# Kernel optimization log

Hardware: AMD Instinct MI355X
Metric: run time of the kernel (lower is better)

## Reference

```python
import jax, jax.numpy as jnp
import numpy as np

HIDDEN = 1024
D_MEM = 256
BATCH = 4
SEQ = 1024
EPS = 1e-6


def elu_plus_one(x):
    # F.elu(x) + 1 == exp(x) for x<0, x+1 for x>=0 (positive feature map)
    return jnp.where(x > 0, x + 1.0, jnp.exp(x))


def setup_inputs() -> dict:
    key = jax.random.key(0)
    ks = jax.random.split(key, 8)
    hidden_states = jax.random.normal(ks[0], (BATCH, SEQ, HIDDEN), dtype=jnp.float32)
    s = 1.0 / np.sqrt(HIDDEN)
    w_q = jax.random.normal(ks[1], (D_MEM, HIDDEN), dtype=jnp.float32) * s
    w_k = jax.random.normal(ks[2], (D_MEM, HIDDEN), dtype=jnp.float32) * s
    w_v = jax.random.normal(ks[3], (D_MEM, HIDDEN), dtype=jnp.float32) * s
    w_o = jax.random.normal(ks[4], (HIDDEN, D_MEM), dtype=jnp.float32) * (1.0 / np.sqrt(D_MEM))
    gate = jnp.zeros((1,), dtype=jnp.float32)
    # nonzero persistent memory state so retrieval path is exercised
    memory = jax.random.normal(ks[5], (D_MEM, D_MEM), dtype=jnp.float32) * 0.1
    memory_norm = jax.random.uniform(ks[6], (D_MEM,), dtype=jnp.float32) * 10.0 + 1.0
    return {
        "hidden_states": hidden_states,
        "w_q": w_q, "w_k": w_k, "w_v": w_v, "w_o": w_o,
        "gate": gate, "memory": memory, "memory_norm": memory_norm,
    }


def _retrieve(sigma_x, memory, memory_norm):
    # [b,s,d] @ [d,d] -> [b,s,d], normalized by sigma_x @ memory_norm
    a_unnorm = jnp.matmul(sigma_x, memory)
    norm = jnp.clip(jnp.matmul(sigma_x, memory_norm), EPS, None)[..., None]
    out = a_unnorm / norm
    # torch: if memory_norm.sum() < 1e-6 -> zeros
    return jnp.where(memory_norm.sum() < EPS, jnp.zeros_like(out), out)


def reference(hidden_states, w_q, w_k, w_v, w_o, gate, memory, memory_norm):
    b, s, _ = hidden_states.shape
    q = jnp.einsum('bsh,dh->bsd', hidden_states, w_q)
    k = jnp.einsum('bsh,dh->bsd', hidden_states, w_k)
    v = jnp.einsum('bsh,dh->bsd', hidden_states, w_v)

    sigma_q = elu_plus_one(q)
    sigma_k = elu_plus_one(k)

    # --- retrieval from compressive memory ---
    memory_output = _retrieve(sigma_q, memory, memory_norm)

    # --- causal linear attention within segment (cumsum form, as in source) ---
    kv = jnp.einsum('bsd,bse->bsde', sigma_k, v)          # [b,s,d,d]
    kv_cumsum = jnp.cumsum(kv, axis=1)                     # [b,s,d,d]
    k_cumsum = jnp.cumsum(sigma_k, axis=1)                 # [b,s,d]
    numerator = jnp.einsum('bsd,bsde->bse', sigma_q, kv_cumsum)
    denominator = jnp.clip(jnp.einsum('bsd,bsd->bs', sigma_q, k_cumsum), EPS, None)[..., None]
    local_output = numerator / denominator

    g = jax.nn.sigmoid(gate[0])
    combined = g * memory_output + (1.0 - g) * local_output
    output = jnp.einsum('bsd,hd->bsh', combined, w_o)

    # --- delta-rule memory update (detached in torch) ---
    retrieved_unnorm = jnp.matmul(sigma_k, memory)
    norm = jnp.clip(jnp.matmul(sigma_k, memory_norm), EPS, None)[..., None]
    delta_v = v - retrieved_unnorm / norm
    memory_update = jnp.einsum('bsd,bse->de', sigma_k, delta_v) / (b * s)
    new_memory = jax.lax.stop_gradient(memory + memory_update)
    z_update = sigma_k.sum(axis=(0, 1)) / b
    new_memory_norm = jax.lax.stop_gradient(memory_norm + z_update)

    return output, new_memory, new_memory_norm
```

## Files before the change

kernel.cpp:

```cpp
#include <hip/hip_runtime.h>


#define HIDDEN 1024
#define DMEM 256
#define BATCH 4
#define SEQ 1024
#define MTOT (BATCH * SEQ)
#define CHUNK 128
#define NCH (SEQ / CHUNK)
#define NCHT (BATCH * NCH)
#define EPSF 1e-6f

typedef __bf16 bf16x8 __attribute__((ext_vector_type(8)));
typedef __bf16 bf16x4 __attribute__((ext_vector_type(4)));
typedef float f32x4 __attribute__((ext_vector_type(4)));

#define GL_LDS(g, l)                                                                   \
  __builtin_amdgcn_global_load_lds((const __attribute__((address_space(1))) void*)(g), \
                                   (__attribute__((address_space(3))) void*)(l), 16, 0, 0)

__device__ __forceinline__ float elu1(float x) { return x > 0.f ? x + 1.f : __expf(x); }

__device__ __forceinline__ void stage128(const __bf16* p, long ld, int k0, __bf16* sm,
                                         int wave) {
// ... 15 lines not shown
    stage128(aptr, lda, k0, smA, wave);
    stage128(bptr, ldb, k0, smB, wave);
    __syncthreads();
#pragma unroll
    for (int h = 0; h < 2; ++h) {
      bf16x8 aF[4], bF[4];
#pragma unroll
      for (int i = 0; i < 4; ++i)
        aF[i] = *reinterpret_cast<const bf16x8*>(smA + h * 4096 +
                                                 (wr * 64 + i * 16 + l16) * 32 + quad * 8);
#pragma unroll
      for (int j = 0; j < 4; ++j)
        bF[j] = *reinterpret_cast<const bf16x8*>(smB + h * 4096 +
                                                 (wc * 64 + j * 16 + l16) * 32 + quad * 8);
#pragma unroll
      for (int i = 0; i < 4; ++i)
#pragma unroll
        for (int j = 0; j < 4; ++j)
          acc[i][j] = __builtin_amdgcn_mfma_f32_16x16x32_bf16(aF[i], bF[j], acc[i][j], 0, 0, 0);
    }
    __syncthreads();
  }
}

__device__ __forceinline__ void gemm64_bk64(const __bf16* aptr, const __bf16* bptr, long ldb,
                                            int klen, __bf16* smA, __bf16* smB, int wave,
                                            int wr, int wc, int quad, int l16,
                                            f32x4 (&acc)[2][4]) {
  for (int k0 = 0; k0 < klen; k0 += 64) {
    stage64(aptr, k0, smA, wave);
    stage128(bptr, ldb, k0, smB, wave);
    __syncthreads();
#pragma unroll
    for (int h = 0; h < 2; ++h) {
      bf16x8 aF[2], bF[4];
#pragma unroll
      for (int i = 0; i < 2; ++i)
        aF[i] = *reinterpret_cast<const bf16x8*>(smA + h * 2048 +
                                                 (wr * 32 + i * 16 + l16) * 32 + quad * 8);
#pragma unroll
      for (int j = 0; j < 4; ++j)
        bF[j] = *reinterpret_cast<const bf16x8*>(smB + h * 4096 +
                                                 (wc * 64 + j * 16 + l16) * 32 + quad * 8);
#pragma unroll
      for (int i = 0; i < 2; ++i)
#pragma unroll
        for (int j = 0; j < 4; ++j)
          acc[i][j] = __builtin_amdgcn_mfma_f32_16x16x32_bf16(aF[i], bF[j], acc[i][j], 0, 0, 0);
    }
    __syncthreads();
  }
}

__global__ void kprep(const float* __restrict__ hs, const float* __restrict__ wq,
                      const float* __restrict__ wk, const float* __restrict__ wv,
                      const float* __restrict__ wo, const float* __restrict__ mem,
                      __bf16* __restrict__ hsb, __bf16* __restrict__ wqkvb,
                      __bf16* __restrict__ wob, __bf16* __restrict__ memT,
                      float* __restrict__ out) {
  __shared__ float s[64][65];
  int b = blockIdx.x, tid = threadIdx.x;
  if (b < 4096) {
    int i = b * 256 + tid;
    float4 f = reinterpret_cast<const float4*>(hs)[i];
    bf16x4 h = {(__bf16)f.x, (__bf16)f.y, (__bf16)f.z, (__bf16)f.w};
    reinterpret_cast<bf16x4*>(hsb)[i] = h;
  } else if (b < 5120) {
    int y = (b - 4096) >> 8;
    const float* src = (y == 0) ? wq : (y == 1) ? wk : (y == 2) ? wv : wo;
    __bf16* dst = (y < 3) ? wqkvb + (size_t)y * (DMEM * HIDDEN) : wob;
    int i = ((b - 4096) & 255) * 256 + tid;
    float4 f = reinterpret_cast<const float4*>(src)[i];
    bf16x4 h = {(__bf16)f.x, (__bf16)f.y, (__bf16)f.z, (__bf16)f.w};
    reinterpret_cast<bf16x4*>(dst)[i] = h;
  } else if (b < 5136) {
    int t = b - 5120;
    int bx = t & 3, by = t >> 2;
    int r0 = tid >> 6, col = tid & 63;
#pragma unroll
    for (int it = 0; it < 16; ++it) {
      int row = it * 4 + r0;
      s[row][col] = mem[(size_t)(by * 64 + row) * DMEM + bx * 64 + col];
    }
    __syncthreads();
#pragma unroll
    for (int it = 0; it < 16; ++it) {
      int row = it * 4 + r0;
      memT[(size_t)(bx * 64 + row) * DMEM + by * 64 + col] = (__bf16)s[col][row];
    }
  } else {
    int g = (b - 5136) * 256 + tid;
    reinterpret_cast<float4*>(out + (size_t)MTOT * HIDDEN)[g] =
        reinterpret_cast<const float4*>(mem)[g];
  }
}

__global__ __launch_bounds__(256) void k1_qkv_mfma(
    const __bf16* __restrict__ X, const __bf16* __restrict__ W, __bf16* __restrict__ sqb,
    __bf16* __restrict__ skb, __bf16* __restrict__ skT, __bf16* __restrict__ vT) {
  __shared__ __bf16 As[4096];
  __shared__ __bf16 Bs[8192];
  int tid = threadIdx.x;
  int lane = tid & 63, wave = tid >> 6;
  int m0 = blockIdx.x * 64;
  int by = blockIdx.y;
  int wsel = by >> 1, n0 = (by & 1) * 128;
  const __bf16* aptr = X + (size_t)(m0 + (tid >> 2)) * HIDDEN + ((tid & 3) << 3);
  const __bf16* bptr = W + (size_t)(by * 128 + (tid >> 2)) * HIDDEN + ((tid & 3) << 3);
  int wr = wave >> 1, wc = wave & 1, quad = lane >> 4, l16 = lane & 15;
  f32x4 acc[2][4] = {};
  gemm64_bk64(aptr, bptr, HIDDEN, HIDDEN, As, Bs, wave, wr, wc, quad, l16, acc);
#pragma unroll
  for (int i = 0; i < 2; ++i)
#pragma unroll
    for (int j = 0; j < 4; ++j) {
      int mb = m0 + wr * 32 + i * 16 + quad * 4;
      int n = n0 + wc * 64 + j * 16 + l16;
      if (wsel == 0) {
#pragma unroll
        for (int r = 0; r < 4; ++r) sqb[(size_t)(mb + r) * DMEM + n] = (__bf16)elu1(acc[i][j][r]);
      } else if (wsel == 1) {
        bf16x4 t;
#pragma unroll
        for (int r = 0; r < 4; ++r) {
          float v = elu1(acc[i][j][r]);
          skb[(size_t)(mb + r) * DMEM + n] = (__bf16)v;
          t[r] = (__bf16)v;
        }
        *reinterpret_cast<bf16x4*>(skT + (size_t)n * MTOT + mb) = t;
      } else {
        bf16x4 t;
#pragma unroll
        for (int r = 0; r < 4; ++r) t[r] = (__bf16)acc[i][j][r];
        *reinterpret_cast<bf16x4*>(vT + (size_t)n * MTOT + mb) = t;
      }
    }
}

__global__ __launch_bounds__(256) void kC(const __bf16* __restrict__ vT,
                                          const __bf16* __restrict__ skT,
                                          const __bf16* __restrict__ sqb,
                                          const __bf16* __restrict__ skb,
                                          __bf16* __restrict__ kvcT, __bf16* __restrict__ scb,
                                          float* __restrict__ ksc) {
  __shared__ __bf16 As[4096];
  __shared__ __bf16 Bs[8192];
  int tid = threadIdx.x;
  int c = blockIdx.x;
  int y = blockIdx.y;
  if (y == 10) {
    int d = tid;
    float s = 0.f;
    for (int i = 0; i < CHUNK; ++i) s += (float)skb[(size_t)(c * CHUNK + i) * DMEM + d];
    ksc[c * DMEM + d] = s;
    return;
  }
  int lane = tid & 63, wave = tid >> 6;
  int wr = wave >> 1, wc = wave & 1, quad = lane >> 4, l16 = lane & 15;
  if (y < 8) {
    int e0 = (y >> 1) * 64, d0 = (y & 1) * 128;
    const __bf16* aptr = vT + (size_t)(e0 + (tid >> 2)) * MTOT + c * CHUNK + ((tid & 3) << 3);
    const __bf16* bptr = skT + (size_t)(d0 + (tid >> 2)) * MTOT + c * CHUNK + ((tid & 3) << 3);
    f32x4 acc[2][4] = {};
    gemm64_bk64(aptr, bptr, MTOT, CHUNK, As, Bs, wave, wr, wc, quad, l16, acc);
#pragma unroll
    for (int i = 0; i < 2; ++i)
#pragma unroll
      for (int j = 0; j < 4; ++j)
#pragma unroll
        for (int r = 0; r < 4; ++r) {
          int e = e0 + wr * 32 + i * 16 + quad * 4 + r;
          int d = d0 + wc * 64 + j * 16 + l16;
          kvcT[(size_t)c * DMEM * DMEM + (size_t)e * DMEM + d] = (__bf16)acc[i][j][r];
        }
  } else {
    int i0 = (y - 8) * 64;
    const __bf16* aptr = sqb + (size_t)(c * CHUNK + i0 + (tid >> 2)) * DMEM + ((tid & 3) << 3);
    const __bf16* bptr = skb + (size_t)(c * CHUNK + (tid >> 2)) * DMEM + ((tid & 3) << 3);
    f32x4 acc[2][4] = {};
    gemm64_bk64(aptr, bptr, DMEM, DMEM, As, Bs, wave, wr, wc, quad, l16, acc);
#pragma unroll
    for (int i = 0; i < 2; ++i)
#pragma unroll
      for (int j = 0; j < 4; ++j)
#pragma unroll
        for (int r = 0; r < 4; ++r) {
          int ii = i0 + wr * 32 + i * 16 + quad * 4 + r;
          int jj = wc * 64 + j * 16 + l16;
          scb[(size_t)c * CHUNK * CHUNK + (size_t)ii * CHUNK + jj] =
              (jj <= ii) ? (__bf16)acc[i][j][r] : (__bf16)0.f;
        }
  }
}

__global__ __launch_bounds__(256) void kD(const __bf16* __restrict__ kvcT,
                                          __bf16* __restrict__ kvpT,
                                          const float* __restrict__ ksc,
                                          const __bf16* __restrict__ scb,
                                          const __bf16* __restrict__ sqb,
                                          const __bf16* __restrict__ skb,
                                          const float* __restrict__ mnorm,
                                          float* __restrict__ den, float* __restrict__ qn,
                                          float* __restrict__ kn) {
  int vt = blockIdx.x;
  int tid = threadIdx.x;
  if (vt < 128) {
    int batch = vt >> 5;
    size_t idx8 = (size_t)(((vt & 31) * 256 + tid)) * 8;
    float run[8] = {};
    for (int c = 0; c < NCH; ++c) {
      size_t off = (size_t)(batch * NCH + c) * DMEM * DMEM + idx8;
      bf16x8 t = *reinterpret_cast<const bf16x8*>(kvcT + off);
      bf16x8 o;
#pragma unroll
      for (int r = 0; r < 8; ++r) o[r] = (__bf16)run[r];
      *reinterpret_cast<bf16x8*>(kvpT + off) = o;
#pragma unroll
      for (int r = 0; r < 8; ++r) run[r] += (float)t[r];
    }
  } else {
    int wave = tid >> 6, lane = tid & 63;
    int m = (vt - 128) * 4 + wave;
    int c = m >> 7;
    int i = m & 127;
    int cb = c & ~7;
    float s_sc = 0.f, s_d2 = 0.f, s_qn = 0.f, s_kn = 0.f;
    for (int j = lane; j < CHUNK; j += 64)
      s_sc += (float)scb[(size_t)c * CHUNK * CHUNK + (size_t)i * CHUNK + j];
    for (int d = lane; d < DMEM; d += 64) {
      float q = (float)sqb[(size_t)m * DMEM + d];
      float k = (float)skb[(size_t)m * DMEM + d];
      float kp = 0.f;
      for (int cc = cb; cc < c; ++cc) kp += ksc[cc * DMEM + d];
      s_d2 += q * kp;
      s_qn += q * mnorm[d];
      s_kn += k * mnorm[d];
    }
#pragma unroll
    for (int off = 32; off > 0; off >>= 1) {
      s_sc += __shfl_down(s_sc, off);
      s_d2 += __shfl_down(s_d2, off);
      s_qn += __shfl_down(s_qn, off);
      s_kn += __shfl_down(s_kn, off);
    }
    if (lane == 0) {
      den[m] = s_sc + s_d2;
      qn[m] = s_qn;
      kn[m] = s_kn;
    }
  }
}

__global__ __launch_bounds__(256) void kE(const __bf16* __restrict__ scb,
                                          const __bf16* __restrict__ sqb,
                                          const __bf16* __restrict__ skb,
                                          const __bf16* __restrict__ vT,
                                          const __bf16* __restrict__ kvpT,
                                          const __bf16* __restrict__ memT,
                                          const float* __restrict__ den,
                                          const float* __restrict__ qn,
                                          const float* __restrict__ kn,
                                          const float* __restrict__ gate,
                                          const float* __restrict__ mnorm,
                                          __bf16* __restrict__ combb, __bf16* __restrict__ dvT) {
  __shared__ __bf16 As[4096];
  __shared__ __bf16 B1s[8192];
  __shared__ __bf16 B2s[8192];
  __shared__ float warr[4];
  int tid = threadIdx.x;
  int lane = tid & 63, wave = tid >> 6;
  int wr = wave >> 1, wc = wave & 1, quad = lane >> 4, l16 = lane & 15;
  int bid = blockIdx.x;
  if (bid < 128) {
    float mv = mnorm[tid];
#pragma unroll
    for (int off = 32; off > 0; off >>= 1) mv += __shfl_down(mv, off);
    if (lane == 0) warr[wave] = mv;
    __syncthreads();
    float fl = ((warr[0] + warr[1] + warr[2] + warr[3]) < EPSF) ? 0.f : 1.f;
    __syncthreads();
    int c = bid >> 2, yy = bid & 3;
    int i0 = (yy >> 1) * 64, e0 = (yy & 1) * 128;
    f32x4 acc_loc[2][4] = {};
    f32x4 acc_mem[2][4] = {};
    {
      const __bf16* aptr =
          scb + (size_t)c * CHUNK * CHUNK + (size_t)(i0 + (tid >> 2)) * CHUNK + ((tid & 3) << 3);
      const __bf16* bptr = vT + (size_t)(e0 + (tid >> 2)) * MTOT + c * CHUNK + ((tid & 3) << 3);
      gemm64_bk64(aptr, bptr, MTOT, CHUNK, As, B1s, wave, wr, wc, quad, l16, acc_loc);
    }
    {
      const __bf16* aptr = sqb + (size_t)(c * CHUNK + i0 + (tid >> 2)) * DMEM + ((tid & 3) << 3);
      const __bf16* b1ptr =
          kvpT + (size_t)c * DMEM * DMEM + (size_t)(e0 + (tid >> 2)) * DMEM + ((tid & 3) << 3);
      const __bf16* b2ptr = memT + (size_t)(e0 + (tid >> 2)) * DMEM + ((tid & 3) << 3);
      for (int k0 = 0; k0 < DMEM; k0 += 64) {
        stage64(aptr, k0, As, wave);
        stage128(b1ptr, DMEM, k0, B1s, wave);
        stage128(b2ptr, DMEM, k0, B2s, wave);
        __syncthreads();
#pragma unroll
        for (int h = 0; h < 2; ++h) {
          bf16x8 aF[2], b1F[4], b2F[4];
#pragma unroll
          for (int i = 0; i < 2; ++i)
            aF[i] = *reinterpret_cast<const bf16x8*>(As + h * 2048 +
                                                     (wr * 32 + i * 16 + l16) * 32 + quad * 8);
#pragma unroll
          for (int j = 0; j < 4; ++j) {
            b1F[j] = *reinterpret_cast<const bf16x8*>(B1s + h * 4096 +
                                                      (wc * 64 + j * 16 + l16) * 32 + quad * 8);
            b2F[j] = *reinterpret_cast<const bf16x8*>(B2s + h * 4096 +
                                                      (wc * 64 + j * 16 + l16) * 32 + quad * 8);
          }
#pragma unroll
          for (int i = 0; i < 2; ++i)
#pragma unroll
            for (int j = 0; j < 4; ++j) {
              acc_loc[i][j] =
                  __builtin_amdgcn_mfma_f32_16x16x32_bf16(aF[i], b1F[j], acc_loc[i][j], 0, 0, 0);
              acc_mem[i][j] =
                  __builtin_amdgcn_mfma_f32_16x16x32_bf16(aF[i], b2F[j], acc_mem[i][j], 0, 0, 0);
            }
        }
        __syncthreads();
      }
    }
    float g = 1.f / (1.f + __expf(-gate[0]));
#pragma unroll
    for (int i = 0; i < 2; ++i) {
      int mb = c * CHUNK + i0 + wr * 32 + i * 16 + quad * 4;
      float dn[4], qv[4];
#pragma unroll
      for (int r = 0; r < 4; ++r) {
        dn[r] = fmaxf(den[mb + r], EPSF);
        qv[r] = fmaxf(qn[mb + r], EPSF);
      }
#pragma unroll
      for (int j = 0; j < 4; ++j) {
        int e = e0 + wc * 64 + j * 16 + l16;
#pragma unroll
        for (int r = 0; r < 4; ++r) {
          float comb = g * fl * acc_mem[i][j][r] / qv[r] + (1.f - g) * acc_loc[i][j][r] / dn[r];
          combb[(size_t)(mb + r) * DMEM + e] = (__bf16)comb;
        }
      }
    }
  } else {
    int t = bid - 128;
    int m0 = (t >> 1) * 64, n0 = (t & 1) * 128;
    const __bf16* aptr = skb + (size_t)(m0 + (tid >> 2)) * DMEM + ((tid & 3) << 3);
    const __bf16* bptr = memT + (size_t)(n0 + (tid >> 2)) * DMEM + ((tid & 3) << 3);
    f32x4 acc[2][4] = {};
    gemm64_bk64(aptr, bptr, DMEM, DMEM, As, B1s, wave, wr, wc, quad, l16, acc);
#pragma unroll
    for (int i = 0; i < 2; ++i) {
      int mb = m0 + wr * 32 + i * 16 + quad * 4;
      float kv[4];
#pragma unroll
      for (int r = 0; r < 4; ++r) kv[r] = fmaxf(kn[mb + r], EPSF);
#pragma unroll
      for (int j = 0; j < 4; ++j) {
        int n = n0 + wc * 64 + j * 16 + l16;
        bf16x4 vv = *reinterpret_cast<const bf16x4*>(vT + (size_t)n * MTOT + mb);
        bf16x4 tt;
#pragma unroll
        for (int r = 0; r < 4; ++r) tt[r] = (__bf16)((float)vv[r] - acc[i][j][r] / kv[r]);
        *reinterpret_cast<bf16x4*>(dvT + (size_t)n * MTOT + mb) = tt;
      }
    }
  }
}

__global__ __launch_bounds__(256) void kF(const __bf16* __restrict__ combb,
                                          const __bf16* __restrict__ wob,
                                          const __bf16* __restrict__ skT,
                                          const __bf16* __restrict__ dvT,
                                          const float* __restrict__ ksc,
                                          const float* __restrict__ mnorm,
                                          float* __restrict__ out) {
  __shared__ __bf16 As[8192];
  __shared__ __bf16 Bs[8192];
  int tid = threadIdx.x;
  int bid = blockIdx.x;
  if (bid == 384) {
    int d = tid;
    float s = 0.f;
    for (int c = 0; c < NCHT; ++c) s += ksc[c * DMEM + d];
    out[(size_t)MTOT * HIDDEN + DMEM * DMEM + d] = mnorm[d] + s * (1.f / (float)BATCH);
    return;
  }
  int lane = tid & 63, wave = tid >> 6;
  int wr = wave >> 1, wc = wave & 1, quad = lane >> 4, l16 = lane & 15;
  if (bid < 256) {
    int m0 = (bid & 31) * 128, by = bid >> 5;
    const __bf16* aptr = combb + (size_t)(m0 + (tid >> 2)) * DMEM + ((tid & 3) << 3);
    const __bf16* bptr = wob + (size_t)(by * 128 + (tid >> 2)) * DMEM + ((tid & 3) << 3);
    f32x4 acc[4][4] = {};
    gemm128_bk64(aptr, DMEM, bptr, DMEM, DMEM, As, Bs, wave, wr, wc, quad, l16, acc);
#pragma unroll
    for (int i = 0; i < 4; ++i)
#pragma unroll
      for (int j = 0; j < 4; ++j)
#pragma unroll
        for (int r = 0; r < 4; ++r) {
          int m = m0 + wr * 64 + i * 16 + quad * 4 + r;
          int n = by * 128 + wc * 64 + j * 16 + l16;
          out[(size_t)m * HIDDEN + n] = acc[i][j][r];
        }
  } else {
    int t = bid - 256;
    int kbase = (t >> 3) * 256;
    int yy = t & 7;
    int d0 = (yy >> 1) * 64, e0 = (yy & 1) * 128;
    const __bf16* aptr = skT + (size_t)(d0 + (tid >> 2)) * MTOT + kbase + ((tid & 3) << 3);
    const __bf16* bptr = dvT + (size_t)(e0 + (tid >> 2)) * MTOT + kbase + ((tid & 3) << 3);
    f32x4 acc[2][4] = {};
    gemm64_bk64(aptr, bptr, MTOT, 256, As, Bs, wave, wr, wc, quad, l16, acc);
    float* base = out + (size_t)MTOT * HIDDEN;
#pragma unroll
    for (int i = 0; i < 2; ++i)
#pragma unroll
      for (int j = 0; j < 4; ++j)
#pragma unroll
        for (int r = 0; r < 4; ++r) {
          int d = d0 + wr * 32 + i * 16 + quad * 4 + r;
          int e = e0 + wc * 64 + j * 16 + l16;
          atomicAdd(&base[(size_t)d * DMEM + e], acc[i][j][r] * (1.f / (float)MTOT));
        }
  }
}

extern "C" void kernel_launch(void* const* d_in, const int* in_sizes, int n_in,
                              void* d_out, int out_size, void* d_ws, size_t ws_size,
                              hipStream_t stream) {
  const float* hs = (const float*)d_in[0];
  const float* wq = (const float*)d_in[1];
  const float* wk = (const float*)d_in[2];
  const float* wv = (const float*)d_in[3];
  const float* wo = (const float*)d_in[4];
  const float* gate = (const float*)d_in[5];
  const float* mem = (const float*)d_in[6];
  const float* mnorm = (const float*)d_in[7];
  float* out = (float*)d_out;
  float* ws = (float*)d_ws;

  float* ksc = ws;
  float* den = ksc + 8192;
  float* qn = den + 4096;
  float* kn = qn + 4096;
  __bf16* kvcT = (__bf16*)(ws + 20480);
  __bf16* hsb = kvcT + (size_t)NCHT * DMEM * DMEM;
  __bf16* wqkvb = hsb + (size_t)MTOT * HIDDEN;
  __bf16* wob = wqkvb + (size_t)3 * DMEM * HIDDEN;
  __bf16* memT = wob + (size_t)HIDDEN * DMEM;
  __bf16* sqb = memT + (size_t)DMEM * DMEM;
  __bf16* skb = sqb + (size_t)MTOT * DMEM;
  __bf16* skT = skb + (size_t)MTOT * DMEM;
  __bf16* vT = skT + (size_t)MTOT * DMEM;
  __bf16* scb = vT + (size_t)MTOT * DMEM;
  __bf16* kvpT = scb + (size_t)NCHT * CHUNK * CHUNK;
  __bf16* combb = kvpT + (size_t)NCHT * DMEM * DMEM;
  __bf16* dvT = combb + (size_t)MTOT * DMEM;

  kprep<<<dim3(5152), 256, 0, stream>>>(hs, wq, wk, wv, wo, mem, hsb, wqkvb, wob, memT, out);
  k1_qkv_mfma<<<dim3(64, 6), 256, 0, stream>>>(hsb, wqkvb, sqb, skb, skT, vT);
  kC<<<dim3(NCHT, 11), 256, 0, stream>>>(vT, skT, sqb, skb, kvcT, scb, ksc);
  kD<<<dim3(1152), 256, 0, stream>>>(kvcT, kvpT, ksc, scb, sqb, skb, mnorm, den, qn, kn);
  kE<<<dim3(256), 256, 0, stream>>>(scb, sqb, skb, vT, kvpT, memT, den, qn, kn, gate, mnorm,
                                    combb, dvT);
  kF<<<dim3(385), 256, 0, stream>>>(combb, wob, skT, dvT, ksc, mnorm, out);
}
```

Before: 139.2 us.

## Fuse scan and normalizer kernels into neighbours, drop kvp prefix buffer

Removes the separate prefix-scan/denominator kernel. The delta-v computation (with its k-norm reduction done in shared memory) moves into the chunk kernel. The retrieval kernel now computes its own denominators and accumulates prior chunk KV products via repeated GEMMs over earlier chunks instead of reading a precomputed prefix. The memory-update GEMM moves into the retrieval launch, and the output projection becomes its own kernel. This cuts one launch and the global round trips for den/qn/kn/kvpT, but adds redundant per-block reductions and up to seven extra GEMMs for late chunks. The kprep grid size also changes.

```diff
diff --git a/kernel.cpp b/kernel.cpp
--- a/kernel.cpp
+++ b/kernel.cpp
@@ -176,14 +176,17 @@
     }
 }
 
-__global__ __launch_bounds__(256) void kC(const __bf16* __restrict__ vT,
-                                          const __bf16* __restrict__ skT,
-                                          const __bf16* __restrict__ sqb,
-                                          const __bf16* __restrict__ skb,
-                                          __bf16* __restrict__ kvcT, __bf16* __restrict__ scb,
-                                          float* __restrict__ ksc) {
+__global__ __launch_bounds__(256) void kC2(const __bf16* __restrict__ vT,
+                                           const __bf16* __restrict__ skT,
+                                           const __bf16* __restrict__ sqb,
+                                           const __bf16* __restrict__ skb,
+                                           const __bf16* __restrict__ memT,
+                                           const float* __restrict__ mnorm,
+                                           __bf16* __restrict__ kvcT, __bf16* __restrict__ scb,
+                                           float* __restrict__ ksc, __bf16* __restrict__ dvT) {
   __shared__ __bf16 As[4096];
   __shared__ __bf16 Bs[8192];
+  __shared__ float knl[64];
   int tid = threadIdx.x;
   int c = blockIdx.x;
   int y = blockIdx.y;
@@ -212,7 +215,7 @@
           int d = d0 + wc * 64 + j * 16 + l16;
           kvcT[(size_t)c * DMEM * DMEM + (size_t)e * DMEM + d] = (__bf16)acc[i][j][r];
         }
-  } else {
+  } else if (y < 10) {
     int i0 = (y - 8) * 64;
     const __bf16* aptr = sqb + (size_t)(c * CHUNK + i0 + (tid >> 2)) * DMEM + ((tid & 3) << 3);
     const __bf16* bptr = skb + (size_t)(c * CHUNK + (tid >> 2)) * DMEM + ((tid & 3) << 3);
@@ -229,87 +232,69 @@
           scb[(size_t)c * CHUNK * CHUNK + (size_t)ii * CHUNK + jj] =
               (jj <= ii) ? (__bf16)acc[i][j][r] : (__bf16)0.f;
         }
-  }
-}
-
-__global__ __launch_bounds__(256) void kD(const __bf16* __restrict__ kvcT,
-                                          __bf16* __restrict__ kvpT,
-                                          const float* __restrict__ ksc,
-                                          const __bf16* __restrict__ scb,
-                                          const __bf16* __restrict__ sqb,
-                                          const __bf16* __restrict__ skb,
-                                          const float* __restrict__ mnorm,
-                                          float* __restrict__ den, float* __restrict__ qn,
-                                          float* __restrict__ kn) {
-  int vt = blockIdx.x;
-  int tid = threadIdx.x;
-  if (vt < 128) {
-    int batch = vt >> 5;
-    size_t idx8 = (size_t)(((vt & 31) * 256 + tid)) * 8;
-    float run[8] = {};
-    for (int c = 0; c < NCH; ++c) {
-      size_t off = (size_t)(batch * NCH + c) * DMEM * DMEM + idx8;
-      bf16x8 t = *reinterpret_cast<const bf16x8*>(kvcT + off);
-      bf16x8 o;
-#pragma unroll
-      for (int r = 0; r < 8; ++r) o[r] = (__bf16)run[r];
-      *reinterpret_cast<bf16x8*>(kvpT + off) = o;
-#pragma unroll
-      for (int r = 0; r < 8; ++r) run[r] += (float)t[r];
-    }
   } else {
-    int wave = tid >> 6, lane = tid & 63;
-    int m = (vt - 128) * 4 + wave;
-    int c = m >> 7;
-    int i = m & 127;
-    int cb = c & ~7;
-    float s_sc = 0.f, s_d2 = 0.f, s_qn = 0.f, s_kn = 0.f;
-    for (int j = lane; j < CHUNK; j += 64)
-      s_sc += (float)scb[(size_t)c * CHUNK * CHUNK + (size_t)i * CHUNK + j];
-    for (int d = lane; d < DMEM; d += 64) {
-      float q = (float)sqb[(size_t)m * DMEM + d];
-      float k = (float)skb[(size_t)m * DMEM + d];
-      float kp = 0.f;
-      for (int cc = cb; cc < c; ++cc) kp += ksc[cc * DMEM + d];
-      s_d2 += q * kp;
-      s_qn += q * mnorm[d];
-      s_kn += k * mnorm[d];
-    }
-#pragma unroll
-    for (int off = 32; off > 0; off >>= 1) {
-      s_sc += __shfl_down(s_sc, off);
-      s_d2 += __shfl_down(s_d2, off);
-      s_qn += __shfl_down(s_qn, off);
-      s_kn += __shfl_down(s_kn, off);
-    }
-    if (lane == 0) {
-      den[m] = s_sc + s_d2;
-      qn[m] = s_qn;
-      kn[m] = s_kn;
-    }
-  }
-}
-
-__global__ __launch_bounds__(256) void kE(const __bf16* __restrict__ scb,
-                                          const __bf16* __restrict__ sqb,
-                                          const __bf16* __restrict__ skb,
-                                          const __bf16* __restrict__ vT,
-                                          const __bf16* __restrict__ kvpT,
-                                          const __bf16* __restrict__ memT,
-                                          const float* __restrict__ den,
-                                          const float* __restrict__ qn,
-                                          const float* __restrict__ kn,
-                                          const float* __restrict__ gate,
-                                          const float* __restrict__ mnorm,
-                                          __bf16* __restrict__ combb, __bf16* __restrict__ dvT) {
+    int t = (y - 11) * 32 + c;
+    int m0 = (t >> 1) * 64, n0 = (t & 1) * 128;
+    for (int rr = 0; rr < 16; ++rr) {
+      int m = m0 + wave * 16 + rr;
+      float s = 0.f;
+      for (int d = lane; d < DMEM; d += 64) s += (float)skb[(size_t)m * DMEM + d] * mnorm[d];
+#pragma unroll
+      for (int off = 32; off > 0; off >>= 1) s += __shfl_down(s, off);
+      if (lane == 0) knl[wave * 16 + rr] = s;
+    }
+    __syncthreads();
+    const __bf16* aptr = skb + (size_t)(m0 + (tid >> 2)) * DMEM + ((tid & 3) << 3);
+    const __bf16* bptr = memT + (size_t)(n0 + (tid >> 2)) * DMEM + ((tid & 3) << 3);
+    f32x4 acc[2][4] = {};
+    gemm64_bk64(aptr, bptr, DMEM, DMEM, As, Bs, wave, wr, wc, quad, l16, acc);
+#pragma unroll
+    for (int i = 0; i < 2; ++i) {
+      int rel = wr * 32 + i * 16 + quad * 4;
+      float kv[4];
+#pragma unroll
+      for (int r = 0; r < 4; ++r) kv[r] = fmaxf(knl[rel + r], EPSF);
+#pragma unroll
+      for (int j = 0; j < 4; ++j) {
+        int n = n0 + wc * 64 + j * 16 + l16;
+        bf16x4 vv = *reinterpret_cast<const bf16x4*>(vT + (size_t)n * MTOT + m0 + rel);
+        bf16x4 tt;
+#pragma unroll
+        for (int r = 0; r < 4; ++r) tt[r] = (__bf16)((float)vv[r] - acc[i][j][r] / kv[r]);
+        *reinterpret_cast<bf16x4*>(dvT + (size_t)n * MTOT + m0 + rel) = tt;
+      }
+    }
+  }
+}
+
+__global__ __launch_bounds__(256) void kE2(const __bf16* __restrict__ scb,
+                                           const __bf16* __restrict__ sqb,
+                                           const __bf16* __restrict__ vT,
+                                           const __bf16* __restrict__ kvcT,
+                                           const __bf16* __restrict__ memT,
+                                           const __bf16* __restrict__ skT,
+                                           const __bf16* __restrict__ dvT,
+                                           const float* __restrict__ ksc,
+                                           const float* __restrict__ gate,
+                                           const float* __restrict__ mnorm,
+                                           __bf16* __restrict__ combb,
+                                           float* __restrict__ out) {
   __shared__ __bf16 As[4096];
-  __shared__ __bf16 B1s[8192];
-  __shared__ __bf16 B2s[8192];
+  __shared__ __bf16 Bs[8192];
+  __shared__ float denl[64];
+  __shared__ float qnl[64];
   __shared__ float warr[4];
   int tid = threadIdx.x;
+  int bid = blockIdx.x;
   int lane = tid & 63, wave = tid >> 6;
   int wr = wave >> 1, wc = wave & 1, quad = lane >> 4, l16 = lane & 15;
-  int bid = blockIdx.x;
+  if (bid == 256) {
+    int d = tid;
+    float s = 0.f;
+    for (int c = 0; c < NCHT; ++c) s += ksc[c * DMEM + d];
+    out[(size_t)MTOT * HIDDEN + DMEM * DMEM + d] = mnorm[d] + s * (1.f / (float)BATCH);
+    return;
+  }
   if (bid < 128) {
     float mv = mnorm[tid];
 #pragma unroll
@@ -317,63 +302,62 @@
     if (lane == 0) warr[wave] = mv;
     __syncthreads();
     float fl = ((warr[0] + warr[1] + warr[2] + warr[3]) < EPSF) ? 0.f : 1.f;
-    __syncthreads();
     int c = bid >> 2, yy = bid & 3;
     int i0 = (yy >> 1) * 64, e0 = (yy & 1) * 128;
+    int cb = c & ~7;
+    for (int rr = 0; rr < 16; ++rr) {
+      int row = wave * 16 + rr;
+      int m = c * CHUNK + i0 + row;
+      float s_sc = 0.f, s_d2 = 0.f, s_qn = 0.f;
+      for (int j = lane; j < CHUNK; j += 64)
+        s_sc += (float)scb[(size_t)c * CHUNK * CHUNK + (size_t)(i0 + row) * CHUNK + j];
+      for (int d = lane; d < DMEM; d += 64) {
+        float q = (float)sqb[(size_t)m * DMEM + d];
+        float kp = 0.f;
+        for (int cc = cb; cc < c; ++cc) kp += ksc[cc * DMEM + d];
+        s_d2 += q * kp;
+        s_qn += q * mnorm[d];
+      }
+#pragma unroll
+      for (int off = 32; off > 0; off >>= 1) {
+        s_sc += __shfl_down(s_sc, off);
+        s_d2 += __shfl_down(s_d2, off);
+        s_qn += __shfl_down(s_qn, off);
+      }
+      if (lane == 0) {
+        denl[row] = s_sc + s_d2;
+        qnl[row] = s_qn;
+      }
+    }
+    __syncthreads();
     f32x4 acc_loc[2][4] = {};
     f32x4 acc_mem[2][4] = {};
     {
       const __bf16* aptr =
           scb + (size_t)c * CHUNK * CHUNK + (size_t)(i0 + (tid >> 2)) * CHUNK + ((tid & 3) << 3);
       const __bf16* bptr = vT + (size_t)(e0 + (tid >> 2)) * MTOT + c * CHUNK + ((tid & 3) << 3);
-      gemm64_bk64(aptr, bptr, MTOT, CHUNK, As, B1s, wave, wr, wc, quad, l16, acc_loc);
+      gemm64_bk64(aptr, bptr, MTOT, CHUNK, As, Bs, wave, wr, wc, quad, l16, acc_loc);
+    }
+    const __bf16* aq = sqb + (size_t)(c * CHUNK + i0 + (tid >> 2)) * DMEM + ((tid & 3) << 3);
+    for (int j = cb; j < c; ++j) {
+      const __bf16* bj =
+          kvcT + (size_t)j * DMEM * DMEM + (size_t)(e0 + (tid >> 2)) * DMEM + ((tid & 3) << 3);
+      gemm64_bk64(aq, bj, DMEM, DMEM, As, Bs, wave, wr, wc, quad, l16, acc_loc);
     }
     {
-      const __bf16* aptr = sqb + (size_t)(c * CHUNK + i0 + (tid >> 2)) * DMEM + ((tid & 3) << 3);
-      const __bf16* b1ptr =
-          kvpT + (size_t)c * DMEM * DMEM + (size_t)(e0 + (tid >> 2)) * DMEM + ((tid & 3) << 3);
-      const __bf16* b2ptr = memT + (size_t)(e0 + (tid >> 2)) * DMEM + ((tid & 3) << 3);
-      for (int k0 = 0; k0 < DMEM; k0 += 64) {
-        stage64(aptr, k0, As, wave);
-        stage128(b1ptr, DMEM, k0, B1s, wave);
-        stage128(b2ptr, DMEM, k0, B2s, wave);
-        __syncthreads();
-#pragma unroll
-        for (int h = 0; h < 2; ++h) {
-          bf16x8 aF[2], b1F[4], b2F[4];
-#pragma unroll
-          for (int i = 0; i < 2; ++i)
-            aF[i] = *reinterpret_cast<const bf16x8*>(As + h * 2048 +
-                                                     (wr * 32 + i * 16 + l16) * 32 + quad * 8);
-#pragma unroll
-          for (int j = 0; j < 4; ++j) {
-            b1F[j] = *reinterpret_cast<const bf16x8*>(B1s + h * 4096 +
-                                                      (wc * 64 + j * 16 + l16) * 32 + quad * 8);
-            b2F[j] = *reinterpret_cast<const bf16x8*>(B2s + h * 4096 +
-                                                      (wc * 64 + j * 16 + l16) * 32 + quad * 8);
-          }
-#pragma unroll
-          for (int i = 0; i < 2; ++i)
-#pragma unroll
-            for (int j = 0; j < 4; ++j) {
-              acc_loc[i][j] =
-                  __builtin_amdgcn_mfma_f32_16x16x32_bf16(aF[i], b1F[j], acc_loc[i][j], 0, 0, 0);
-              acc_mem[i][j] =
-                  __builtin_amdgcn_mfma_f32_16x16x32_bf16(aF[i], b2F[j], acc_mem[i][j], 0, 0, 0);
-            }
-        }
-        __syncthreads();
-      }
+      const __bf16* bm = memT + (size_t)(e0 + (tid >> 2)) * DMEM + ((tid & 3) << 3);
+      gemm64_bk64(aq, bm, DMEM, DMEM, As, Bs, wave, wr, wc, quad, l16, acc_mem);
     }
     float g = 1.f / (1.f + __expf(-gate[0]));
 #pragma unroll
     for (int i = 0; i < 2; ++i) {
-      int mb = c * CHUNK + i0 + wr * 32 + i * 16 + quad * 4;
+      int rel = wr * 32 + i * 16 + quad * 4;
+      int mb = c * CHUNK + i0 + rel;
       float dn[4], qv[4];
 #pragma unroll
       for (int r = 0; r < 4; ++r) {
-        dn[r] = fmaxf(den[mb + r], EPSF);
-        qv[r] = fmaxf(qn[mb + r], EPSF);
+        dn[r] = fmaxf(denl[rel + r], EPSF);
+        qv[r] = fmaxf(qnl[rel + r], EPSF);
       }
 #pragma unroll
       for (int j = 0; j < 4; ++j) {
@@ -387,68 +371,6 @@
     }
   } else {
     int t = bid - 128;
-    int m0 = (t >> 1) * 64, n0 = (t & 1) * 128;
-    const __bf16* aptr = skb + (size_t)(m0 + (tid >> 2)) * DMEM + ((tid & 3) << 3);
-    const __bf16* bptr = memT + (size_t)(n0 + (tid >> 2)) * DMEM + ((tid & 3) << 3);
-    f32x4 acc[2][4] = {};
-    gemm64_bk64(aptr, bptr, DMEM, DMEM, As, B1s, wave, wr, wc, quad, l16, acc);
-#pragma unroll
-    for (int i = 0; i < 2; ++i) {
-      int mb = m0 + wr * 32 + i * 16 + quad * 4;
-      float kv[4];
-#pragma unroll
-      for (int r = 0; r < 4; ++r) kv[r] = fmaxf(kn[mb + r], EPSF);
-#pragma unroll
-      for (int j = 0; j < 4; ++j) {
-        int n = n0 + wc * 64 + j * 16 + l16;
-        bf16x4 vv = *reinterpret_cast<const bf16x4*>(vT + (size_t)n * MTOT + mb);
-        bf16x4 tt;
-#pragma unroll
-        for (int r = 0; r < 4; ++r) tt[r] = (__bf16)((float)vv[r] - acc[i][j][r] / kv[r]);
-        *reinterpret_cast<bf16x4*>(dvT + (size_t)n * MTOT + mb) = tt;
-      }
-    }
-  }
-}
-
-__global__ __launch_bounds__(256) void kF(const __bf16* __restrict__ combb,
-                                          const __bf16* __restrict__ wob,
-                                          const __bf16* __restrict__ skT,
-                                          const __bf16* __restrict__ dvT,
-                                          const float* __restrict__ ksc,
-                                          const float* __restrict__ mnorm,
-                                          float* __restrict__ out) {
-  __shared__ __bf16 As[8192];
-  __shared__ __bf16 Bs[8192];
-  int tid = threadIdx.x;
-  int bid = blockIdx.x;
-  if (bid == 384) {
-    int d = tid;
-    float s = 0.f;
-    for (int c = 0; c < NCHT; ++c) s += ksc[c * DMEM + d];
-    out[(size_t)MTOT * HIDDEN + DMEM * DMEM + d] = mnorm[d] + s * (1.f / (float)BATCH);
-    return;
-  }
-  int lane = tid & 63, wave = tid >> 6;
-  int wr = wave >> 1, wc = wave & 1, quad = lane >> 4, l16 = lane & 15;
-  if (bid < 256) {
-    int m0 = (bid & 31) * 128, by = bid >> 5;
-    const __bf16* aptr = combb + (size_t)(m0 + (tid >> 2)) * DMEM + ((tid & 3) << 3);
-    const __bf16* bptr = wob + (size_t)(by * 128 + (tid >> 2)) * DMEM + ((tid & 3) << 3);
-    f32x4 acc[4][4] = {};
-    gemm128_bk64(aptr, DMEM, bptr, DMEM, DMEM, As, Bs, wave, wr, wc, quad, l16, acc);
-#pragma unroll
-    for (int i = 0; i < 4; ++i)
-#pragma unroll
-      for (int j = 0; j < 4; ++j)
-#pragma unroll
-        for (int r = 0; r < 4; ++r) {
-          int m = m0 + wr * 64 + i * 16 + quad * 4 + r;
-          int n = by * 128 + wc * 64 + j * 16 + l16;
-          out[(size_t)m * HIDDEN + n] = acc[i][j][r];
-        }
-  } else {
-    int t = bid - 256;
     int kbase = (t >> 3) * 256;
     int yy = t & 7;
     int d0 = (yy >> 1) * 64, e0 = (yy & 1) * 128;
@@ -468,6 +390,32 @@
           atomicAdd(&base[(size_t)d * DMEM + e], acc[i][j][r] * (1.f / (float)MTOT));
         }
   }
+}
+
+__global__ __launch_bounds__(256) void kF2(const __bf16* __restrict__ combb,
+                                           const __bf16* __restrict__ wob,
+                                           float* __restrict__ out) {
+  __shared__ __bf16 As[8192];
+  __shared__ __bf16 Bs[8192];
+  int tid = threadIdx.x;
+  int bid = blockIdx.x;
+  int lane = tid & 63, wave = tid >> 6;
+  int wr = wave >> 1, wc = wave & 1, quad = lane >> 4, l16 = lane & 15;
+  int m0 = (bid & 31) * 128, by = bid >> 5;
+  const __bf16* aptr = combb + (size_t)(m0 + (tid >> 2)) * DMEM + ((tid & 3) << 3);
+  const __bf16* bptr = wob + (size_t)(by * 128 + (tid >> 2)) * DMEM + ((tid & 3) << 3);
+  f32x4 acc[4][4] = {};
+  gemm128_bk64(aptr, DMEM, bptr, DMEM, DMEM, As, Bs, wave, wr, wc, quad, l16, acc);
+#pragma unroll
+  for (int i = 0; i < 4; ++i)
+#pragma unroll
+    for (int j = 0; j < 4; ++j)
+#pragma unroll
+      for (int r = 0; r < 4; ++r) {
+        int m = m0 + wr * 64 + i * 16 + quad * 4 + r;
+        int n = by * 128 + wc * 64 + j * 16 + l16;
+        out[(size_t)m * HIDDEN + n] = acc[i][j][r];
+      }
 }
 
 extern "C" void kernel_launch(void* const* d_in, const int* in_sizes, int n_in,
@@ -485,9 +433,6 @@
   float* ws = (float*)d_ws;
 
   float* ksc = ws;
-  float* den = ksc + 8192;
-  float* qn = den + 4096;
-  float* kn = qn + 4096;
   __bf16* kvcT = (__bf16*)(ws + 20480);
   __bf16* hsb = kvcT + (size_t)NCHT * DMEM * DMEM;
   __bf16* wqkvb = hsb + (size_t)MTOT * HIDDEN;
@@ -502,11 +447,10 @@
   __bf16* combb = kvpT + (size_t)NCHT * DMEM * DMEM;
   __bf16* dvT = combb + (size_t)MTOT * DMEM;
 
-  kprep<<<dim3(5152), 256, 0, stream>>>(hs, wq, wk, wv, wo, mem, hsb, wqkvb, wob, memT, out);
+  kprep<<<dim3(5200), 256, 0, stream>>>(hs, wq, wk, wv, wo, mem, hsb, wqkvb, wob, memT, out);
   k1_qkv_mfma<<<dim3(64, 6), 256, 0, stream>>>(hsb, wqkvb, sqb, skb, skT, vT);
-  kC<<<dim3(NCHT, 11), 256, 0, stream>>>(vT, skT, sqb, skb, kvcT, scb, ksc);
-  kD<<<dim3(1152), 256, 0, stream>>>(kvcT, kvpT, ksc, scb, sqb, skb, mnorm, den, qn, kn);
-  kE<<<dim3(256), 256, 0, stream>>>(scb, sqb, skb, vT, kvpT, memT, den, qn, kn, gate, mnorm,
-                                    combb, dvT);
-  kF<<<dim3(385), 256, 0, stream>>>(combb, wob, skT, dvT, ksc, mnorm, out);
-}
+  kC2<<<dim3(NCHT, 15), 256, 0, stream>>>(vT, skT, sqb, skb, memT, mnorm, kvcT, scb, ksc, dvT);
+  kE2<<<dim3(257), 256, 0, stream>>>(scb, sqb, vT, kvcT, memT, skT, dvT, ksc, gate, mnorm,
+                                     combb, out);
+  kF2<<<dim3(256), 256, 0, stream>>>(combb, wob, out);
+}
```

Result: slower. 238.6 us (+71.4%).

## Rebalance kernel stages: move delta-v GEMM earlier, memory-update GEMM alongside retrieval

Applied to the files above, without the earlier changes.

The delta-v computation (sigma_k @ memory and the normalization) moves from kE into kC2 as extra blocks. It now computes the k-norm per row locally in shared memory instead of reading it from kD. The memory-update atomic GEMM and the norm update move from kF into kE3, so they run alongside the combine blocks, and kF3 keeps only the output projection. kprep and kD are coarsened to fewer blocks, each with more work per thread. The aim is better balance of work across the launched kernels and fewer tiny blocks, at the cost of more heterogeneous blocks per kernel.

```diff
diff --git a/kernel.cpp b/kernel.cpp
--- a/kernel.cpp
+++ b/kernel.cpp
@@ -91,29 +91,44 @@
   }
 }
 
-__global__ void kprep(const float* __restrict__ hs, const float* __restrict__ wq,
-                      const float* __restrict__ wk, const float* __restrict__ wv,
-                      const float* __restrict__ wo, const float* __restrict__ mem,
-                      __bf16* __restrict__ hsb, __bf16* __restrict__ wqkvb,
-                      __bf16* __restrict__ wob, __bf16* __restrict__ memT,
-                      float* __restrict__ out) {
+__global__ __launch_bounds__(256) void kprep2(
+    const float* __restrict__ hs, const float* __restrict__ wq, const float* __restrict__ wk,
+    const float* __restrict__ wv, const float* __restrict__ wo, const float* __restrict__ mem,
+    __bf16* __restrict__ hsb, __bf16* __restrict__ wqkvb, __bf16* __restrict__ wob,
+    __bf16* __restrict__ memT, float* __restrict__ out) {
   __shared__ float s[64][65];
   int b = blockIdx.x, tid = threadIdx.x;
-  if (b < 4096) {
-    int i = b * 256 + tid;
-    float4 f = reinterpret_cast<const float4*>(hs)[i];
-    bf16x4 h = {(__bf16)f.x, (__bf16)f.y, (__bf16)f.z, (__bf16)f.w};
-    reinterpret_cast<bf16x4*>(hsb)[i] = h;
-  } else if (b < 5120) {
-    int y = (b - 4096) >> 8;
-    const float* src = (y == 0) ? wq : (y == 1) ? wk : (y == 2) ? wv : wo;
-    __bf16* dst = (y < 3) ? wqkvb + (size_t)y * (DMEM * HIDDEN) : wob;
-    int i = ((b - 4096) & 255) * 256 + tid;
-    float4 f = reinterpret_cast<const float4*>(src)[i];
-    bf16x4 h = {(__bf16)f.x, (__bf16)f.y, (__bf16)f.z, (__bf16)f.w};
-    reinterpret_cast<bf16x4*>(dst)[i] = h;
-  } else if (b < 5136) {
-    int t = b - 5120;
+  if (b < 256) {
+#pragma unroll
+    for (int it = 0; it < 16; ++it) {
+      int i = b * 4096 + it * 256 + tid;
+      float4 f = reinterpret_cast<const float4*>(hs)[i];
+      bf16x4 h = {(__bf16)f.x, (__bf16)f.y, (__bf16)f.z, (__bf16)f.w};
+      reinterpret_cast<bf16x4*>(hsb)[i] = h;
+    }
+  } else if (b < 304) {
+    int t = b - 256;
+    int mat = t >> 4;
+    const float* src = (mat == 0) ? wq : (mat == 1) ? wk : wv;
+    __bf16* dst = wqkvb + (size_t)mat * (DMEM * HIDDEN);
+#pragma unroll
+    for (int it = 0; it < 16; ++it) {
+      int i = (t & 15) * 4096 + it * 256 + tid;
+      float4 f = reinterpret_cast<const float4*>(src)[i];
+      bf16x4 h = {(__bf16)f.x, (__bf16)f.y, (__bf16)f.z, (__bf16)f.w};
+      reinterpret_cast<bf16x4*>(dst)[i] = h;
+    }
+  } else if (b < 320) {
+    int t = b - 304;
+#pragma unroll
+    for (int it = 0; it < 16; ++it) {
+      int i = t * 4096 + it * 256 + tid;
+      float4 f = reinterpret_cast<const float4*>(wo)[i];
+      bf16x4 h = {(__bf16)f.x, (__bf16)f.y, (__bf16)f.z, (__bf16)f.w};
+      reinterpret_cast<bf16x4*>(wob)[i] = h;
+    }
+  } else if (b < 336) {
+    int t = b - 320;
     int bx = t & 3, by = t >> 2;
     int r0 = tid >> 6, col = tid & 63;
 #pragma unroll
@@ -128,9 +143,13 @@
       memT[(size_t)(bx * 64 + row) * DMEM + by * 64 + col] = (__bf16)s[col][row];
     }
   } else {
-    int g = (b - 5136) * 256 + tid;
-    reinterpret_cast<float4*>(out + (size_t)MTOT * HIDDEN)[g] =
-        reinterpret_cast<const float4*>(mem)[g];
+    int t = b - 336;
+#pragma unroll
+    for (int it = 0; it < 4; ++it) {
+      int g = t * 1024 + it * 256 + tid;
+      reinterpret_cast<float4*>(out + (size_t)MTOT * HIDDEN)[g] =
+          reinterpret_cast<const float4*>(mem)[g];
+    }
   }
 }
 
@@ -176,14 +195,17 @@
     }
 }
 
-__global__ __launch_bounds__(256) void kC(const __bf16* __restrict__ vT,
-                                          const __bf16* __restrict__ skT,
-                                          const __bf16* __restrict__ sqb,
-                                          const __bf16* __restrict__ skb,
-                                          __bf16* __restrict__ kvcT, __bf16* __restrict__ scb,
-                                          float* __restrict__ ksc) {
+__global__ __launch_bounds__(256) void kC2(const __bf16* __restrict__ vT,
+                                           const __bf16* __restrict__ skT,
+                                           const __bf16* __restrict__ sqb,
+                                           const __bf16* __restrict__ skb,
+                                           const __bf16* __restrict__ memT,
+                                           const float* __restrict__ mnorm,
+                                           __bf16* __restrict__ kvcT, __bf16* __restrict__ scb,
+                                           float* __restrict__ ksc, __bf16* __restrict__ dvT) {
   __shared__ __bf16 As[4096];
   __shared__ __bf16 Bs[8192];
+  __shared__ float knl[64];
   int tid = threadIdx.x;
   int c = blockIdx.x;
   int y = blockIdx.y;
@@ -212,7 +234,7 @@
           int d = d0 + wc * 64 + j * 16 + l16;
           kvcT[(size_t)c * DMEM * DMEM + (size_t)e * DMEM + d] = (__bf16)acc[i][j][r];
         }
-  } else {
+  } else if (y < 10) {
     int i0 = (y - 8) * 64;
     const __bf16* aptr = sqb + (size_t)(c * CHUNK + i0 + (tid >> 2)) * DMEM + ((tid & 3) << 3);
     const __bf16* bptr = skb + (size_t)(c * CHUNK + (tid >> 2)) * DMEM + ((tid & 3) << 3);
@@ -229,23 +251,53 @@
           scb[(size_t)c * CHUNK * CHUNK + (size_t)ii * CHUNK + jj] =
               (jj <= ii) ? (__bf16)acc[i][j][r] : (__bf16)0.f;
         }
-  }
-}
-
-__global__ __launch_bounds__(256) void kD(const __bf16* __restrict__ kvcT,
-                                          __bf16* __restrict__ kvpT,
-                                          const float* __restrict__ ksc,
-                                          const __bf16* __restrict__ scb,
-                                          const __bf16* __restrict__ sqb,
-                                          const __bf16* __restrict__ skb,
-                                          const float* __restrict__ mnorm,
-                                          float* __restrict__ den, float* __restrict__ qn,
-                                          float* __restrict__ kn) {
-  int vt = blockIdx.x;
+  } else {
+    int t = (y - 11) * 32 + c;
+    int m0 = (t >> 1) * 64, n0 = (t & 1) * 128;
+    for (int rr = 0; rr < 16; ++rr) {
+      int m = m0 + wave * 16 + rr;
+      float s = 0.f;
+      for (int d = lane; d < DMEM; d += 64) s += (float)skb[(size_t)m * DMEM + d] * mnorm[d];
+#pragma unroll
+      for (int off = 32; off > 0; off >>= 1) s += __shfl_down(s, off);
+      if (lane == 0) knl[wave * 16 + rr] = s;
+    }
+    __syncthreads();
+    const __bf16* aptr = skb + (size_t)(m0 + (tid >> 2)) * DMEM + ((tid & 3) << 3);
+    const __bf16* bptr = memT + (size_t)(n0 + (tid >> 2)) * DMEM + ((tid & 3) << 3);
+    f32x4 acc[2][4] = {};
+    gemm64_bk64(aptr, bptr, DMEM, DMEM, As, Bs, wave, wr, wc, quad, l16, acc);
+#pragma unroll
+    for (int i = 0; i < 2; ++i) {
+      int rel = wr * 32 + i * 16 + quad * 4;
+      float kv[4];
+#pragma unroll
+      for (int r = 0; r < 4; ++r) kv[r] = fmaxf(knl[rel + r], EPSF);
+#pragma unroll
+      for (int j = 0; j < 4; ++j) {
+        int n = n0 + wc * 64 + j * 16 + l16;
+        bf16x4 vv = *reinterpret_cast<const bf16x4*>(vT + (size_t)n * MTOT + m0 + rel);
+        bf16x4 tt;
+#pragma unroll
+        for (int r = 0; r < 4; ++r) tt[r] = (__bf16)((float)vv[r] - acc[i][j][r] / kv[r]);
+        *reinterpret_cast<bf16x4*>(dvT + (size_t)n * MTOT + m0 + rel) = tt;
+      }
+    }
+  }
+}
+
+__global__ __launch_bounds__(256) void kD2(const __bf16* __restrict__ kvcT,
+                                           __bf16* __restrict__ kvpT,
+                                           const float* __restrict__ ksc,
+                                           const __bf16* __restrict__ scb,
+                                           const __bf16* __restrict__ sqb,
+                                           const float* __restrict__ mnorm,
+                                           float* __restrict__ den, float* __restrict__ qn) {
+  int bid = blockIdx.x;
   int tid = threadIdx.x;
-  if (vt < 128) {
-    int batch = vt >> 5;
-    size_t idx8 = (size_t)(((vt & 31) * 256 + tid)) * 8;
+  if (bid < 128) {
+    int batch = bid >> 5;
+    size_t idx8 = (size_t)(((bid & 31) * 256 + tid)) * 8;
     float run[8] = {};
     for (int c = 0; c < NCH; ++c) {
       size_t off = (size_t)(batch * NCH + c) * DMEM * DMEM + idx8;
@@ -259,57 +311,62 @@
     }
   } else {
     int wave = tid >> 6, lane = tid & 63;
-    int m = (vt - 128) * 4 + wave;
-    int c = m >> 7;
-    int i = m & 127;
-    int cb = c & ~7;
-    float s_sc = 0.f, s_d2 = 0.f, s_qn = 0.f, s_kn = 0.f;
-    for (int j = lane; j < CHUNK; j += 64)
-      s_sc += (float)scb[(size_t)c * CHUNK * CHUNK + (size_t)i * CHUNK + j];
-    for (int d = lane; d < DMEM; d += 64) {
-      float q = (float)sqb[(size_t)m * DMEM + d];
-      float k = (float)skb[(size_t)m * DMEM + d];
-      float kp = 0.f;
-      for (int cc = cb; cc < c; ++cc) kp += ksc[cc * DMEM + d];
-      s_d2 += q * kp;
-      s_qn += q * mnorm[d];
-      s_kn += k * mnorm[d];
-    }
-#pragma unroll
-    for (int off = 32; off > 0; off >>= 1) {
-      s_sc += __shfl_down(s_sc, off);
-      s_d2 += __shfl_down(s_d2, off);
-      s_qn += __shfl_down(s_qn, off);
-      s_kn += __shfl_down(s_kn, off);
-    }
-    if (lane == 0) {
-      den[m] = s_sc + s_d2;
-      qn[m] = s_qn;
-      kn[m] = s_kn;
-    }
-  }
-}
-
-__global__ __launch_bounds__(256) void kE(const __bf16* __restrict__ scb,
-                                          const __bf16* __restrict__ sqb,
-                                          const __bf16* __restrict__ skb,
-                                          const __bf16* __restrict__ vT,
-                                          const __bf16* __restrict__ kvpT,
-                                          const __bf16* __restrict__ memT,
-                                          const float* __restrict__ den,
-                                          const float* __restrict__ qn,
-                                          const float* __restrict__ kn,
-                                          const float* __restrict__ gate,
-                                          const float* __restrict__ mnorm,
-                                          __bf16* __restrict__ combb, __bf16* __restrict__ dvT) {
+    int wid = (bid - 128) * 4 + wave;
+    for (int m = wid; m < MTOT; m += 1024) {
+      int c = m >> 7, i = m & 127, cb = c & ~7;
+      float s_sc = 0.f, s_d2 = 0.f, s_qn = 0.f;
+      for (int j = lane; j < CHUNK; j += 64)
+        s_sc += (float)scb[(size_t)c * CHUNK * CHUNK + (size_t)i * CHUNK + j];
+      for (int d = lane; d < DMEM; d += 64) {
+        float q = (float)sqb[(size_t)m * DMEM + d];
+        float kp = 0.f;
+        for (int cc = cb; cc < c; ++cc) kp += ksc[cc * DMEM + d];
+        s_d2 += q * kp;
+        s_qn += q * mnorm[d];
+      }
+#pragma unroll
+      for (int off = 32; off > 0; off >>= 1) {
+        s_sc += __shfl_down(s_sc, off);
+        s_d2 += __shfl_down(s_d2, off);
+        s_qn += __shfl_down(s_qn, off);
+      }
+      if (lane == 0) {
+        den[m] = s_sc + s_d2;
+        qn[m] = s_qn;
+      }
+    }
+  }
+}
+
+__global__ __launch_bounds__(256) void kE3(const __bf16* __restrict__ scb,
+                                           const __bf16* __restrict__ sqb,
+                                           const __bf16* __restrict__ vT,
+                                           const __bf16* __restrict__ kvpT,
+                                           const __bf16* __restrict__ memT,
+                                           const __bf16* __restrict__ skT,
+                                           const __bf16* __restrict__ dvT,
+                                           const float* __restrict__ ksc,
+                                           const float* __restrict__ den,
+                                           const float* __restrict__ qn,
+                                           const float* __restrict__ gate,
+                                           const float* __restrict__ mnorm,
+                                           __bf16* __restrict__ combb,
+                                           float* __restrict__ out) {
   __shared__ __bf16 As[4096];
   __shared__ __bf16 B1s[8192];
   __shared__ __bf16 B2s[8192];
   __shared__ float warr[4];
   int tid = threadIdx.x;
+  int bid = blockIdx.x;
   int lane = tid & 63, wave = tid >> 6;
   int wr = wave >> 1, wc = wave & 1, quad = lane >> 4, l16 = lane & 15;
-  int bid = blockIdx.x;
+  if (bid == 256) {
+    int d = tid;
+    float s = 0.f;
+    for (int c = 0; c < NCHT; ++c) s += ksc[c * DMEM + d];
+    out[(size_t)MTOT * HIDDEN + DMEM * DMEM + d] = mnorm[d] + s * (1.f / (float)BATCH);
+    return;
+  }
   if (bid < 128) {
     float mv = mnorm[tid];
 #pragma unroll
@@ -387,75 +444,13 @@
     }
   } else {
     int t = bid - 128;
-    int m0 = (t >> 1) * 64, n0 = (t & 1) * 128;
-    const __bf16* aptr = skb + (size_t)(m0 + (tid >> 2)) * DMEM + ((tid & 3) << 3);
-    const __bf16* bptr = memT + (size_t)(n0 + (tid >> 2)) * DMEM + ((tid & 3) << 3);
-    f32x4 acc[2][4] = {};
-    gemm64_bk64(aptr, bptr, DMEM, DMEM, As, B1s, wave, wr, wc, quad, l16, acc);
-#pragma unroll
-    for (int i = 0; i < 2; ++i) {
-      int mb = m0 + wr * 32 + i * 16 + quad * 4;
-      float kv[4];
-#pragma unroll
-      for (int r = 0; r < 4; ++r) kv[r] = fmaxf(kn[mb + r], EPSF);
-#pragma unroll
-      for (int j = 0; j < 4; ++j) {
-        int n = n0 + wc * 64 + j * 16 + l16;
-        bf16x4 vv = *reinterpret_cast<const bf16x4*>(vT + (size_t)n * MTOT + mb);
-        bf16x4 tt;
-#pragma unroll
-        for (int r = 0; r < 4; ++r) tt[r] = (__bf16)((float)vv[r] - acc[i][j][r] / kv[r]);
-        *reinterpret_cast<bf16x4*>(dvT + (size_t)n * MTOT + mb) = tt;
-      }
-    }
-  }
-}
-
-__global__ __launch_bounds__(256) void kF(const __bf16* __restrict__ combb,
-                                          const __bf16* __restrict__ wob,
-                                          const __bf16* __restrict__ skT,
-                                          const __bf16* __restrict__ dvT,
-                                          const float* __restrict__ ksc,
-                                          const float* __restrict__ mnorm,
-                                          float* __restrict__ out) {
-  __shared__ __bf16 As[8192];
-  __shared__ __bf16 Bs[8192];
-  int tid = threadIdx.x;
-  int bid = blockIdx.x;
-  if (bid == 384) {
-    int d = tid;
-    float s = 0.f;
-    for (int c = 0; c < NCHT; ++c) s += ksc[c * DMEM + d];
-    out[(size_t)MTOT * HIDDEN + DMEM * DMEM + d] = mnorm[d] + s * (1.f / (float)BATCH);
-    return;
-  }
-  int lane = tid & 63, wave = tid >> 6;
-  int wr = wave >> 1, wc = wave & 1, quad = lane >> 4, l16 = lane & 15;
-  if (bid < 256) {
-    int m0 = (bid & 31) * 128, by = bid >> 5;
-    const __bf16* aptr = combb + (size_t)(m0 + (tid >> 2)) * DMEM + ((tid & 3) << 3);
-    const __bf16* bptr = wob + (size_t)(by * 128 + (tid >> 2)) * DMEM + ((tid & 3) << 3);
-    f32x4 acc[4][4] = {};
-    gemm128_bk64(aptr, DMEM, bptr, DMEM, DMEM, As, Bs, wave, wr, wc, quad, l16, acc);
-#pragma unroll
-    for (int i = 0; i < 4; ++i)
-#pragma unroll
-      for (int j = 0; j < 4; ++j)
-#pragma unroll
-        for (int r = 0; r < 4; ++r) {
-          int m = m0 + wr * 64 + i * 16 + quad * 4 + r;
-          int n = by * 128 + wc * 64 + j * 16 + l16;
-          out[(size_t)m * HIDDEN + n] = acc[i][j][r];
-        }
-  } else {
-    int t = bid - 256;
     int kbase = (t >> 3) * 256;
     int yy = t & 7;
     int d0 = (yy >> 1) * 64, e0 = (yy & 1) * 128;
     const __bf16* aptr = skT + (size_t)(d0 + (tid >> 2)) * MTOT + kbase + ((tid & 3) << 3);
     const __bf16* bptr = dvT + (size_t)(e0 + (tid >> 2)) * MTOT + kbase + ((tid & 3) << 3);
     f32x4 acc[2][4] = {};
-    gemm64_bk64(aptr, bptr, MTOT, 256, As, Bs, wave, wr, wc, quad, l16, acc);
+    gemm64_bk64(aptr, bptr, MTOT, 256, As, B1s, wave, wr, wc, quad, l16, acc);
     float* base = out + (size_t)MTOT * HIDDEN;
 #pragma unroll
     for (int i = 0; i < 2; ++i)
@@ -468,6 +463,32 @@
           atomicAdd(&base[(size_t)d * DMEM + e], acc[i][j][r] * (1.f / (float)MTOT));
         }
   }
+}
+
+__global__ __launch_bounds__(256) void kF3(const __bf16* __restrict__ combb,
+                                           const __bf16* __restrict__ wob,
+                                           float* __restrict__ out) {
+  __shared__ __bf16 As[8192];
+  __shared__ __bf16 Bs[8192];
+  int tid = threadIdx.x;
+  int bid = blockIdx.x;
+  int lane = tid & 63, wave = tid >> 6;
+  int wr = wave >> 1, wc = wave & 1, quad = lane >> 4, l16 = lane & 15;
+  int m0 = (bid & 31) * 128, by = bid >> 5;
+  const __bf16* aptr = combb + (size_t)(m0 + (tid >> 2)) * DMEM + ((tid & 3) << 3);
+  const __bf16* bptr = wob + (size_t)(by * 128 + (tid >> 2)) * DMEM + ((tid & 3) << 3);
+  f32x4 acc[4][4] = {};
+  gemm128_bk64(aptr, DMEM, bptr, DMEM, DMEM, As, Bs, wave, wr, wc, quad, l16, acc);
+#pragma unroll
+  for (int i = 0; i < 4; ++i)
+#pragma unroll
+    for (int j = 0; j < 4; ++j)
+#pragma unroll
+      for (int r = 0; r < 4; ++r) {
+        int m = m0 + wr * 64 + i * 16 + quad * 4 + r;
+        int n = by * 128 + wc * 64 + j * 16 + l16;
+        out[(size_t)m * HIDDEN + n] = acc[i][j][r];
+      }
 }
 
 extern "C" void kernel_launch(void* const* d_in, const int* in_sizes, int n_in,
@@ -488,6 +509,7 @@
   float* den = ksc + 8192;
   float* qn = den + 4096;
   float* kn = qn + 4096;
+  (void)kn;
   __bf16* kvcT = (__bf16*)(ws + 20480);
   __bf16* hsb = kvcT + (size_t)NCHT * DMEM * DMEM;
   __bf16* wqkvb = hsb + (size_t)MTOT * HIDDEN;
@@ -502,11 +524,11 @@
   __bf16* combb = kvpT + (size_t)NCHT * DMEM * DMEM;
   __bf16* dvT = combb + (size_t)MTOT * DMEM;
 
-  kprep<<<dim3(5152), 256, 0, stream>>>(hs, wq, wk, wv, wo, mem, hsb, wqkvb, wob, memT, out);
+  kprep2<<<dim3(352), 256, 0, stream>>>(hs, wq, wk, wv, wo, mem, hsb, wqkvb, wob, memT, out);
   k1_qkv_mfma<<<dim3(64, 6), 256, 0, stream>>>(hsb, wqkvb, sqb, skb, skT, vT);
-  kC<<<dim3(NCHT, 11), 256, 0, stream>>>(vT, skT, sqb, skb, kvcT, scb, ksc);
-  kD<<<dim3(1152), 256, 0, stream>>>(kvcT, kvpT, ksc, scb, sqb, skb, mnorm, den, qn, kn);
-  kE<<<dim3(256), 256, 0, stream>>>(scb, sqb, skb, vT, kvpT, memT, den, qn, kn, gate, mnorm,
-                                    combb, dvT);
-  kF<<<dim3(385), 256, 0, stream>>>(combb, wob, skT, dvT, ksc, mnorm, out);
-}
+  kC2<<<dim3(NCHT, 15), 256, 0, stream>>>(vT, skT, sqb, skb, memT, mnorm, kvcT, scb, ksc, dvT);
+  kD2<<<dim3(384), 256, 0, stream>>>(kvcT, kvpT, ksc, scb, sqb, mnorm, den, qn);
+  kE3<<<dim3(257), 256, 0, stream>>>(scb, sqb, vT, kvpT, memT, skT, dvT, ksc, den, qn, gate,
+                                     mnorm, combb, out);
+  kF3<<<dim3(256), 256, 0, stream>>>(combb, wob, out);
+}
```

New measurement: 169.4 us. 1.22x slower.
